# Performance work log

Hardware: AMD Instinct MI355X
Metric: run time of the kernel (lower is better)

Reference implementation:

```python
import jax, jax.numpy as jnp
import numpy as np

N = 8192          # total neurons (n)
IN_NEURONS = 1024 # input_neurons
OUT_NEURONS = 256 # output_neurons


def setup_inputs() -> dict:
    key = jax.random.key(0)
    k1, k2 = jax.random.split(key)
    x = jax.random.normal(k1, (1, IN_NEURONS), dtype=jnp.float32)
    # learned adjacency weight (original uses kaiming_uniform; scale kept small for stability)
    W = jax.random.normal(k2, (N, N), dtype=jnp.float32) * 0.01
    return {"x": x, "W": W, "num_steps": 4}


def reference(x, W, num_steps):
    n = W.shape[0]
    # load_input_neurons: state = (W.T * pad(x[0], n)).T  ==  W * s0[:, None]
    s0 = jnp.pad(x[0], (0, n - x.shape[1]))        # [n]
    state = W * s0[:, None]                        # [n, n]

    # step(): next = sum_i(W.T * state[i]) then .T  ==  W * colsum(state)[:, None]
    def body(state, _):
        col_sum = state.sum(axis=0)                # [n]
        return W * col_sum[:, None], None

    state, _ = jax.lax.scan(body, state, None, length=num_steps)

    # extract_output_neurons: diagonal entries state[-i, -i], i = OUT..1
    return jnp.diagonal(state)[-OUT_NEURONS:]      # [OUT_NEURONS]
```

## Files before the change

kernel.cpp:

```cpp
#include <hip/hip_runtime.h>


namespace {
constexpr int N = 8192;
constexpr int IN_N = 1024;
constexpr int OUT_N = 256;
}

__global__ void zero_f32(float* __restrict__ p, int n) {
  int i = blockIdx.x * blockDim.x + threadIdx.x;
  if (i < n) p[i] = 0.0f;
}

__global__ void gemv_wt(const float* __restrict__ W,
                        const float* __restrict__ vin,
                        float* __restrict__ vout,
                        int i_chunk) {
  const int j = (blockIdx.x * blockDim.x + threadIdx.x) * 4;
  const int i0 = blockIdx.y * i_chunk;
  const float* __restrict__ wp = W + (size_t)i0 * N + j;
  const float* __restrict__ vp = vin + i0;
  float ax = 0.f, ay = 0.f, az = 0.f, aw = 0.f;
  for (int i = 0; i < i_chunk; ++i) {
    const float s = vp[i];
    const float4 w = *reinterpret_cast<const float4*>(wp);
    ax += w.x * s;
    ay += w.y * s;
    az += w.z * s;
    aw += w.w * s;
    wp += N;
  }
  atomicAdd(vout + j + 0, ax);
  atomicAdd(vout + j + 1, ay);
  atomicAdd(vout + j + 2, az);
  atomicAdd(vout + j + 3, aw);
}

__global__ void gemv_wt_tail(const float* __restrict__ W,
                             const float* __restrict__ vin,
                             float* __restrict__ vout,
                             int i_chunk) {
  const int j = N - OUT_N + threadIdx.x;
  const int i0 = blockIdx.x * i_chunk;
  const float* __restrict__ wp = W + (size_t)i0 * N + j;
  float acc = 0.f;
  for (int i = 0; i < i_chunk; ++i) {
    acc += *wp * vin[i0 + i];
    wp += N;
  }
  atomicAdd(vout + j, acc);
}

__global__ void diag_scale(const float* __restrict__ W,
                           const float* __restrict__ v4,
                           float* __restrict__ out) {
  const int t = threadIdx.x;
  const int j = N - OUT_N + t;
  out[t] = W[(size_t)j * N + j] * v4[j];
}

extern "C" void kernel_launch(void* const* d_in, const int* in_sizes, int n_in,
                              void* d_out, int out_size, void* d_ws, size_t ws_size,
                              hipStream_t stream) {
  const float* x = (const float*)d_in[0];
  const float* W = (const float*)d_in[1];

  float* ws = (float*)d_ws;
  float* v1 = ws;
  float* v2 = ws + N;
  float* v3 = ws + 2 * N;
  float* v4 = ws + 3 * N;
  float* out = (float*)d_out;

  zero_f32<<<(4 * N) / 256, 256, 0, stream>>>(ws, 4 * N);

  {
    dim3 grid(N / (256 * 4), IN_N / 32);
    gemv_wt<<<grid, 256, 0, stream>>>(W, x, v1, 32);
  }
  {
    dim3 grid(N / (256 * 4), N / 128);
    gemv_wt<<<grid, 256, 0, stream>>>(W, v1, v2, 128);
  }
  {
    dim3 grid(N / (256 * 4), N / 128);
    gemv_wt<<<grid, 256, 0, stream>>>(W, v2, v3, 128);
  }
  gemv_wt_tail<<<N / 128, OUT_N, 0, stream>>>(W, v3, v4, 128);

  diag_scale<<<1, OUT_N, 0, stream>>>(W, v4, out);
}
```

Before: 472.2 us.

## Fuse all GEMV stages into one cooperative kernel with partial-sum reduction

Replaces the chain of separate GEMV kernels, each ending in atomic adds, with a single cooperative kernel. The kernel writes per-block partial vectors to workspace and reduces them after grid-wide syncs. This removes launch overhead, the zeroing kernel and heavy atomic contention on the output vectors. In exchange it adds extra global traffic for the partial buffer and several grid barriers, and it requires all 512 blocks to be co-resident.

```diff
diff --git a/kernel.cpp b/kernel.cpp
--- a/kernel.cpp
+++ b/kernel.cpp
@@ -1,62 +1,132 @@
 #include <hip/hip_runtime.h>
+#include <hip/hip_cooperative_groups.h>
+
+namespace cg = cooperative_groups;
 
 
 namespace {
 constexpr int N = 8192;
+constexpr int NF4 = N / 4;
 constexpr int IN_N = 1024;
 constexpr int OUT_N = 256;
+constexpr int GB = 512;
+constexpr int BT = 256;
+constexpr int K4 = NF4 / BT;
+constexpr int CH_MAIN = N / GB;
+constexpr int CH_IN = IN_N / GB;
+constexpr size_t OFF_V1 = 0;
+constexpr size_t OFF_V2 = 8192;
+constexpr size_t OFF_V3 = 16384;
+constexpr size_t OFF_V4 = 24576;
+constexpr size_t OFF_P  = 32768;
 }
 
-__global__ void zero_f32(float* __restrict__ p, int n) {
-  int i = blockIdx.x * blockDim.x + threadIdx.x;
-  if (i < n) p[i] = 0.0f;
+template <int ROWS>
+__device__ inline void gemv_partial(const float* __restrict__ W,
+                                    const float* __restrict__ vin_s,
+                                    float* __restrict__ P,
+                                    int b, int t, int i0) {
+  float4 acc[K4];
+#pragma unroll
+  for (int k = 0; k < K4; ++k) acc[k] = make_float4(0.f, 0.f, 0.f, 0.f);
+#pragma unroll 2
+  for (int i = 0; i < ROWS; ++i) {
+    const float s = vin_s[i];
+    const float4* row = reinterpret_cast<const float4*>(W) + (size_t)(i0 + i) * NF4;
+#pragma unroll
+    for (int k = 0; k < K4; ++k) {
+      const float4 w = row[k * BT + t];
+      acc[k].x += w.x * s;
+      acc[k].y += w.y * s;
+      acc[k].z += w.z * s;
+      acc[k].w += w.w * s;
+    }
+  }
+  float4* Pc = reinterpret_cast<float4*>(P + (size_t)b * N);
+#pragma unroll
+  for (int k = 0; k < K4; ++k) Pc[k * BT + t] = acc[k];
 }
 
-__global__ void gemv_wt(const float* __restrict__ W,
-                        const float* __restrict__ vin,
-                        float* __restrict__ vout,
-                        int i_chunk) {
-  const int j = (blockIdx.x * blockDim.x + threadIdx.x) * 4;
-  const int i0 = blockIdx.y * i_chunk;
-  const float* __restrict__ wp = W + (size_t)i0 * N + j;
-  const float* __restrict__ vp = vin + i0;
-  float ax = 0.f, ay = 0.f, az = 0.f, aw = 0.f;
-  for (int i = 0; i < i_chunk; ++i) {
-    const float s = vp[i];
-    const float4 w = *reinterpret_cast<const float4*>(wp);
-    ax += w.x * s;
-    ay += w.y * s;
-    az += w.z * s;
-    aw += w.w * s;
-    wp += N;
+__device__ inline void reduce_P(const float* __restrict__ P, float* __restrict__ v,
+                                int b, int t, float* lds_r) {
+  const int j = b * 16 + (t & 15);
+  const int c0 = (t >> 4) * 32;
+  float a = 0.f;
+#pragma unroll 8
+  for (int cc = 0; cc < 32; ++cc) a += P[(size_t)(c0 + cc) * N + j];
+  lds_r[t] = a;
+  __syncthreads();
+  if (t < 16) {
+    float s = 0.f;
+#pragma unroll
+    for (int g = 0; g < 16; ++g) s += lds_r[g * 16 + t];
+    v[b * 16 + t] = s;
   }
-  atomicAdd(vout + j + 0, ax);
-  atomicAdd(vout + j + 1, ay);
-  atomicAdd(vout + j + 2, az);
-  atomicAdd(vout + j + 3, aw);
 }
 
-__global__ void gemv_wt_tail(const float* __restrict__ W,
-                             const float* __restrict__ vin,
-                             float* __restrict__ vout,
-                             int i_chunk) {
-  const int j = N - OUT_N + threadIdx.x;
-  const int i0 = blockIdx.x * i_chunk;
-  const float* __restrict__ wp = W + (size_t)i0 * N + j;
-  float acc = 0.f;
-  for (int i = 0; i < i_chunk; ++i) {
-    acc += *wp * vin[i0 + i];
-    wp += N;
+__global__ __launch_bounds__(BT, 4) void fused_adj(const float* __restrict__ W,
+                                                   const float* __restrict__ x,
+                                                   float* __restrict__ ws,
+                                                   float* __restrict__ out) {
+  cg::grid_group grid = cg::this_grid();
+  const int b = blockIdx.x;
+  const int t = threadIdx.x;
+  float* v1 = ws + OFF_V1;
+  float* v2 = ws + OFF_V2;
+  float* v3 = ws + OFF_V3;
+  float* v4 = ws + OFF_V4;
+  float* P  = ws + OFF_P;
+
+  __shared__ float lds_v[CH_MAIN];
+  __shared__ float lds_r[BT];
+
+  if (b == 0 && t < OUT_N) v4[t] = 0.0f;
+
+  gemv_partial<CH_IN>(W, x + b * CH_IN, P, b, t, b * CH_IN);
+  grid.sync();
+  reduce_P(P, v1, b, t, lds_r);
+  grid.sync();
+
+  if (t < CH_MAIN) lds_v[t] = v1[b * CH_MAIN + t];
+  __syncthreads();
+  gemv_partial<CH_MAIN>(W, lds_v, P, b, t, b * CH_MAIN);
+  grid.sync();
+  reduce_P(P, v2, b, t, lds_r);
+  grid.sync();
+
+  if (t < CH_MAIN) lds_v[t] = v2[b * CH_MAIN + t];
+  __syncthreads();
+  gemv_partial<CH_MAIN>(W, lds_v, P, b, t, b * CH_MAIN);
+  grid.sync();
+  reduce_P(P, v3, b, t, lds_r);
+  grid.sync();
+
+  if (t < CH_MAIN) lds_v[t] = v3[b * CH_MAIN + t];
+  __syncthreads();
+  if (t < 64) {
+    const int i0 = b * CH_MAIN;
+    float4 a = make_float4(0.f, 0.f, 0.f, 0.f);
+#pragma unroll 4
+    for (int i = 0; i < CH_MAIN; ++i) {
+      const float4 w =
+          (reinterpret_cast<const float4*>(W) + (size_t)(i0 + i) * NF4)[1984 + t];
+      const float s = lds_v[i];
+      a.x += w.x * s;
+      a.y += w.y * s;
+      a.z += w.z * s;
+      a.w += w.w * s;
+    }
+    atomicAdd(v4 + 4 * t + 0, a.x);
+    atomicAdd(v4 + 4 * t + 1, a.y);
+    atomicAdd(v4 + 4 * t + 2, a.z);
+    atomicAdd(v4 + 4 * t + 3, a.w);
   }
-  atomicAdd(vout + j, acc);
-}
+  grid.sync();
 
-__global__ void diag_scale(const float* __restrict__ W,
-                           const float* __restrict__ v4,
-                           float* __restrict__ out) {
-  const int t = threadIdx.x;
-  const int j = N - OUT_N + t;
-  out[t] = W[(size_t)j * N + j] * v4[j];
+  if (b == 0 && t < OUT_N) {
+    const size_t j = (size_t)(N - OUT_N + t);
+    out[t] = W[j * (N + 1)] * v4[t];
+  }
 }
 
 extern "C" void kernel_launch(void* const* d_in, const int* in_sizes, int n_in,
@@ -64,29 +134,9 @@
                               hipStream_t stream) {
   const float* x = (const float*)d_in[0];
   const float* W = (const float*)d_in[1];
-
   float* ws = (float*)d_ws;
-  float* v1 = ws;
-  float* v2 = ws + N;
-  float* v3 = ws + 2 * N;
-  float* v4 = ws + 3 * N;
   float* out = (float*)d_out;
 
-  zero_f32<<<(4 * N) / 256, 256, 0, stream>>>(ws, 4 * N);
-
-  {
-    dim3 grid(N / (256 * 4), IN_N / 32);
-    gemv_wt<<<grid, 256, 0, stream>>>(W, x, v1, 32);
-  }
-  {
-    dim3 grid(N / (256 * 4), N / 128);
-    gemv_wt<<<grid, 256, 0, stream>>>(W, v1, v2, 128);
-  }
-  {
-    dim3 grid(N / (256 * 4), N / 128);
-    gemv_wt<<<grid, 256, 0, stream>>>(W, v2, v3, 128);
-  }
-  gemv_wt_tail<<<N / 128, OUT_N, 0, stream>>>(W, v3, v4, 128);
-
-  diag_scale<<<1, OUT_N, 0, stream>>>(W, v4, out);
+  void* args[] = {(void*)&W, (void*)&x, (void*)&ws, (void*)&out};
+  hipLaunchCooperativeKernel((void*)fused_adj, dim3(GB), dim3(BT), args, 0, stream);
 }
```

After: 871.8 us. 1.85x slower.
